# Optimization experiments

Measured on AMD Instinct MI355X. Metric: run time of the kernel, lower is better.

## Reference

```python
import jax, jax.numpy as jnp
import numpy as np

INPUT_DIM = 256
NODE_DIM = 6
OUTPUT_DIM = 256
N_NODES = 10000
N_EDGES = 320000


def setup_inputs() -> dict:
    key = jax.random.key(0)
    ks = jax.random.split(key, 6)
    x = jax.random.normal(ks[0], (N_NODES, NODE_DIM), dtype=jnp.float32)
    edge_index = jax.random.randint(ks[1], (2, N_EDGES), 0, N_NODES, dtype=jnp.int64 if jax.config.jax_enable_x64 else jnp.int32)
    edge_attr = jax.random.normal(ks[2], (N_EDGES, INPUT_DIM), dtype=jnp.float32)
    mask = jax.random.uniform(ks[3], (N_EDGES,), dtype=jnp.float32)
    in_feat = INPUT_DIM * 3 + NODE_DIM * 2  # 774
    limit = float(np.sqrt(6.0 / (in_feat + OUTPUT_DIM)))  # xavier_uniform
    W = jax.random.uniform(ks[4], (OUTPUT_DIM, in_feat), dtype=jnp.float32, minval=-limit, maxval=limit)
    b = jax.random.uniform(ks[5], (OUTPUT_DIM,), dtype=jnp.float32, minval=-1.0 / np.sqrt(in_feat), maxval=1.0 / np.sqrt(in_feat))
    return {"x": x, "num_nodes": N_NODES, "edge_index": edge_index, "edge_attr": edge_attr, "mask": mask, "W": W, "b": b}


def reference(x, num_nodes, edge_index, edge_attr, mask, W, b):
    row = edge_index[0]
    col = edge_index[1]
    # masked mean-ish aggregation of edge features into destination nodes
    num = jax.ops.segment_sum(edge_attr * mask[:, None], col, num_segments=num_nodes)  # [N, input_dim]
    den = jax.ops.segment_sum(mask[:, None], col, num_segments=num_nodes)             # [N, 1]
    node_rep = num / (den + 1.0)
    node_rep = jnp.concatenate([node_rep, x], axis=1)  # [N, input_dim + node_dim]
    edge_rep = jnp.concatenate([node_rep[row], node_rep[col], edge_attr], axis=-1)  # [E, 3*input_dim + 2*node_dim]
    edge_rep = edge_rep @ W.T + b  # [E, output_dim]
    return (node_rep, edge_rep)
```

## Files before the change

kernel.cpp:

```cpp
#include <hip/hip_runtime.h>
#include <hip/hip_bf16.h>
#include <stdint.h>

typedef __attribute__((ext_vector_type(4))) float f32x4;
typedef __attribute__((ext_vector_type(8))) short bf16x8;

#define NDIM 6
#define IN_DIM 256
#define OUT_DIM 256
#define KW 780
#define NR 262
#define NRP 320
#define SCAN_T 1024

__device__ __forceinline__ short f2bf(float f) {
  return __builtin_bit_cast(short, __float2bfloat16(f));
}

__device__ __forceinline__ void gload_lds16(void* lds, const void* g) {
  __builtin_amdgcn_global_load_lds(
      (const __attribute__((address_space(1))) unsigned int*)g,
      (__attribute__((address_space(3))) unsigned int*)lds, 16, 0, 0);
}

__global__ void hist_kernel(const int* __restrict__ ei, int* __restrict__ counts, int E) {
  int e = blockIdx.x * 256 + threadIdx.x;
  if (e < E) atomicAdd(&counts[ei[(long)E + e]], 1);
}

__global__ __launch_bounds__(SCAN_T) void scan_kernel(const int* __restrict__ counts,
                                                      int* __restrict__ offsets, int N) {
  __shared__ int part[SCAN_T];
  int t = threadIdx.x;
  int chunk = (N + SCAN_T - 1) / SCAN_T;
  int begin = t * chunk;
  int s = 0;
  for (int i = 0; i < chunk; ++i) {
    int idx = begin + i;
    if (idx < N) s += counts[idx];
  }
  part[t] = s;
  __syncthreads();
  for (int d = 1; d < SCAN_T; d <<= 1) {
    int v = (t >= d) ? part[t - d] : 0;
    __syncthreads();
    part[t] += v;
    __syncthreads();
  }
  int run = (t == 0) ? 0 : part[t - 1];
  for (int i = 0; i < chunk; ++i) {
    int idx = begin + i;
    if (idx < N) { offsets[idx] = run; run += counts[idx]; }
  }
}

__global__ void scatter_kernel(const int* __restrict__ ei, const int* __restrict__ offsets,
                               int* __restrict__ cursor, int* __restrict__ csr, int E) {
  int e = blockIdx.x * 256 + threadIdx.x;
  if (e >= E) return;
  int col = ei[(long)E + e];
  int pos = atomicAdd(&cursor[col], 1);
  csr[offsets[col] + pos] = e;
}

__global__ __launch_bounds__(256) void reduce_kernel(
    const int* __restrict__ csr, const int* __restrict__ offsets,
    const int* __restrict__ counts, const float* __restrict__ ea,
    const float* __restrict__ mask, const float* __restrict__ x,
    float* __restrict__ outN, short* __restrict__ nrepb, int N) {
  int n = blockIdx.x * 4 + (threadIdx.x >> 6);
  if (n >= N) return;
  int lane = threadIdx.x & 63;
  int s = offsets[n], cnt = counts[n];
  f32x4 sum = (f32x4)0.0f;
  float den = 0.0f;
#pragma unroll 4
  for (int i = 0; i < cnt; ++i) {
    int e = csr[s + i];
    float m = mask[e];
    den += m;
    f32x4 v = ((const f32x4*)ea)[(long)e * 64 + lane];
    sum.x += v.x * m; sum.y += v.y * m; sum.z += v.z * m; sum.w += v.w * m;
  }
  float inv = 1.0f / (den + 1.0f);
  sum.x *= inv; sum.y *= inv; sum.z *= inv; sum.w *= inv;
  float* po = outN + (long)n * NR + lane * 4;
  po[0] = sum.x; po[1] = sum.y; po[2] = sum.z; po[3] = sum.w;
  short4 pb;
  pb.x = f2bf(sum.x); pb.y = f2bf(sum.y); pb.z = f2bf(sum.z); pb.w = f2bf(sum.w);
  *(short4*)(nrepb + (long)n * NRP + lane * 4) = pb;
  if (lane < NDIM) {
    float xv = x[(long)n * NDIM + lane];
    outN[(long)n * NR + IN_DIM + lane] = xv;
    nrepb[(long)n * NRP + IN_DIM + lane] = f2bf(xv);
  } else if (lane < 8) {
    nrepb[(long)n * NRP + IN_DIM + lane] = 0;
  }
}

__global__ void wprep_kernel(const float* __restrict__ W, short* __restrict__ Weat,
                             short* __restrict__ Wrt, short* __restrict__ Wct) {
  int idx = blockIdx.x * 256 + threadIdx.x;
  if (idx < OUT_DIM * 256) {
    int n = idx >> 8, k = idx & 255;
    Weat[idx] = f2bf(W[(long)n * KW + 2 * NR + k]);
    return;
  }
  idx -= OUT_DIM * 256;
  if (idx < OUT_DIM * NRP) {
    int n = idx / NRP, k = idx % NRP;
    Wrt[idx] = f2bf(k < NR ? W[(long)n * KW + k] : 0.0f);
    return;
  }
  idx -= OUT_DIM * NRP;
  if (idx < OUT_DIM * NRP) {
    int n = idx / NRP, k = idx % NRP;
    Wct[idx] = f2bf(k < NR ? W[(long)n * KW + NR + k] : 0.0f);
  }
}

__global__ __launch_bounds__(256, 2) void pgemm_kernel(
    const short* __restrict__ nrepb, const short* __restrict__ Wrt,
    const short* __restrict__ Wct, const float* __restrict__ bias,
    float* __restrict__ Pr, float* __restrict__ Pc, int N) {
  __shared__ short As[5][64 * 64];
  const int tid = threadIdx.x;
  const int wave = tid >> 6, lane = tid & 63;
  const int m0 = blockIdx.x * 64;
  const int table = blockIdx.y;
  const short* Wt = table ? Wct : Wrt;
  float* P = table ? Pc : Pr;
  const int nbase = wave * 64;

  float bvals[4];
#pragma unroll
  for (int nf = 0; nf < 4; ++nf)
    bvals[nf] = table ? 0.0f : bias[nbase + 16 * nf + (lane & 15)];

  f32x4 acc[4][4];
#pragma unroll
  for (int mf = 0; mf < 4; ++mf)
#pragma unroll
    for (int nf = 0; nf < 4; ++nf) acc[mf][nf] = (f32x4)0.0f;

  bf16x8 bv[2][8];
  auto loadB = [&](int t, int tb) {
#pragma unroll
    for (int s2 = 0; s2 < 2; ++s2)
#pragma unroll
      for (int nf = 0; nf < 4; ++nf)
        bv[tb][s2 * 4 + nf] = *(const bf16x8*)&Wt[
            (long)(nbase + nf * 16 + (lane & 15)) * NRP + t * 64 + s2 * 32 + (lane >> 4) * 8];
  };

  const int scp = lane & 7;
#pragma unroll
  for (int t = 0; t < 5; ++t)
#pragma unroll
    for (int i = 0; i < 2; ++i) {
      int row = 16 * wave + 8 * i + (lane >> 3);
      int c = scp ^ (row & 7);
      long m = m0 + row; if (m >= N) m = N - 1;
      gload_lds16(&As[t][(16 * wave + 8 * i) * 64], nrepb + m * NRP + t * 64 + 8 * c);
    }
  loadB(0, 0);
  asm volatile("s_waitcnt vmcnt(8)" ::: "memory");
  __builtin_amdgcn_s_barrier();
  __builtin_amdgcn_sched_barrier(0);

#pragma unroll
  for (int t = 0; t < 5; ++t) {
    if (t < 4) loadB(t + 1, (t + 1) & 1);
    if (t < 4) asm volatile("s_waitcnt vmcnt(8)" ::: "memory");
    else       asm volatile("s_waitcnt vmcnt(0)" ::: "memory");
#pragma unroll
    for (int s2 = 0; s2 < 2; ++s2) {
      bf16x8 a[4];
      int cl = s2 * 4 + (lane >> 4);
#pragma unroll
      for (int mf = 0; mf < 4; ++mf) {
        int m = 16 * mf + (lane & 15);
        a[mf] = *(const bf16x8*)&As[t][m * 64 + ((cl ^ (m & 7)) * 8)];
      }
#pragma unroll
      for (int mf = 0; mf < 4; ++mf)
#pragma unroll
        for (int nf = 0; nf < 4; ++nf)
          acc[mf][nf] = __builtin_amdgcn_mfma_f32_16x16x32_bf16(
              a[mf], bv[t & 1][s2 * 4 + nf], acc[mf][nf], 0, 0, 0);
    }
  }

#pragma unroll
  for (int mf = 0; mf < 4; ++mf)
#pragma unroll
    for (int nf = 0; nf < 4; ++nf)
#pragma unroll
      for (int q = 0; q < 4; ++q) {
        long m = m0 + 16 * mf + (lane >> 4) * 4 + q;
        if (m < N)
          P[m * OUT_DIM + nbase + 16 * nf + (lane & 15)] = acc[mf][nf][q] + bvals[nf];
      }
}

__global__ __launch_bounds__(256, 2) void egemm_kernel(
    const int* __restrict__ ei, const float* __restrict__ ea,
    const short* __restrict__ Weat, const float* __restrict__ Pr,
    const float* __restrict__ Pc, float* __restrict__ outE, int E) {
  __shared__ short As[4][64 * 64];
  const int tid = threadIdx.x;
  const int wave = tid >> 6, lane = tid & 63;
  const long e0 = (long)blockIdx.x * 64;
  const int nbase = wave * 64;

  f32x4 acc[4][4];
#pragma unroll
  for (int mf = 0; mf < 4; ++mf)
#pragma unroll
    for (int nf = 0; nf < 4; ++nf) acc[mf][nf] = (f32x4)0.0f;

  bf16x8 bv[2][8];
  auto loadB = [&](int t, int tb) {
#pragma unroll
    for (int s2 = 0; s2 < 2; ++s2)
#pragma unroll
      for (int nf = 0; nf < 4; ++nf)
        bv[tb][s2 * 4 + nf] = *(const bf16x8*)&Weat[
            (nbase + nf * 16 + (lane & 15)) * 256 + t * 64 + s2 * 32 + (lane >> 4) * 8];
  };

  f32x4 eh[8][2];
#pragma unroll
  for (int j = 0; j < 8; ++j) {
    int c8 = tid + j * 256;
    int row = c8 >> 5, cp8 = c8 & 31;
    long e = e0 + row; if (e >= E) e = E - 1;
    const f32x4* s = (const f32x4*)(ea + (e * IN_DIM + cp8 * 8));
    eh[j][0] = s[0];
    eh[j][1] = s[1];
  }
  loadB(0, 0);
  __builtin_amdgcn_sched_barrier(0);
#pragma unroll
  for (int j = 0; j < 8; ++j) {
    int c8 = tid + j * 256;
    int row = c8 >> 5, cp8 = c8 & 31;
    int t = cp8 >> 3, cp = cp8 & 7;
    f32x4 v0 = eh[j][0], v1 = eh[j][1];
    bf16x8 p;
    p[0] = f2bf(v0.x); p[1] = f2bf(v0.y); p[2] = f2bf(v0.z); p[3] = f2bf(v0.w);
    p[4] = f2bf(v1.x); p[5] = f2bf(v1.y); p[6] = f2bf(v1.z); p[7] = f2bf(v1.w);
    *(bf16x8*)&As[t][row * 64 + ((cp ^ (row & 7)) * 8)] = p;
  }
  asm volatile("s_waitcnt lgkmcnt(0)" ::: "memory");
  __builtin_amdgcn_s_barrier();
  __builtin_amdgcn_sched_barrier(0);

#pragma unroll
  for (int t = 0; t < 4; ++t) {
    if (t < 3) loadB(t + 1, (t + 1) & 1);
    if (t < 3) asm volatile("s_waitcnt vmcnt(8)" ::: "memory");
    else       asm volatile("s_waitcnt vmcnt(0)" ::: "memory");
#pragma unroll
    for (int s2 = 0; s2 < 2; ++s2) {
      bf16x8 a[4];
      int cl = s2 * 4 + (lane >> 4);
#pragma unroll
      for (int mf = 0; mf < 4; ++mf) {
        int m = 16 * mf + (lane & 15);
        a[mf] = *(const bf16x8*)&As[t][m * 64 + ((cl ^ (m & 7)) * 8)];
      }
#pragma unroll
      for (int mf = 0; mf < 4; ++mf)
#pragma unroll
        for (int nf = 0; nf < 4; ++nf)
          acc[mf][nf] = __builtin_amdgcn_mfma_f32_16x16x32_bf16(
              a[mf], bv[t & 1][s2 * 4 + nf], acc[mf][nf], 0, 0, 0);
    }
  }

#pragma unroll
  for (int mf = 0; mf < 4; ++mf) {
#pragma unroll
    for (int q = 0; q < 4; ++q) {
      long e = e0 + 16 * mf + (lane >> 4) * 4 + q;
      bool ok = e < E;
      long ec = ok ? e : (E - 1);
      int re = ei[ec], ce = ei[(long)E + ec];
      const float* pr = Pr + (long)re * OUT_DIM;
      const float* pc = Pc + (long)ce * OUT_DIM;
      if (ok) {
#pragma unroll
        for (int nf = 0; nf < 4; ++nf) {
          int n = nbase + 16 * nf + (lane & 15);
          outE[e * OUT_DIM + n] = acc[mf][nf][q] + pr[n] + pc[n];
        }
      }
    }
  }
}

extern "C" void kernel_launch(void* const* d_in, const int* in_sizes, int n_in,
                              void* d_out, int out_size, void* d_ws, size_t ws_size,
                              hipStream_t stream) {
  const float* x    = (const float*)d_in[0];
  const int*   ei   = (const int*)d_in[2];
  const float* ea   = (const float*)d_in[3];
  const float* mask = (const float*)d_in[4];
  const float* W    = (const float*)d_in[5];
  const float* b    = (const float*)d_in[6];
  const int E = in_sizes[4];
  const int N = in_sizes[0] / NDIM;

  char* p = (char*)d_ws;
  int* counts  = (int*)p; p += (long)N * 4;
  int* cursor  = (int*)p; p += (long)N * 4;
  int* offsets = (int*)p; p += (long)(N + 1) * 4;
  int* csr     = (int*)p; p += (long)E * 4;
  p = (char*)(((uintptr_t)p + 15) & ~(uintptr_t)15);
  short* nrepb = (short*)p; p += (long)N * NRP * 2;
  short* Weat  = (short*)p; p += (long)OUT_DIM * 256 * 2;
  short* Wrt   = (short*)p; p += (long)OUT_DIM * NRP * 2;
  short* Wct   = (short*)p; p += (long)OUT_DIM * NRP * 2;
  float* Pr    = (float*)p; p += (long)N * OUT_DIM * 4;
  float* Pc    = (float*)p;

  float* outN = (float*)d_out;
  float* outE = outN + (long)N * NR;

  hipMemsetAsync(counts, 0, (size_t)2 * N * 4, stream);

  hist_kernel<<<(E + 255) / 256, 256, 0, stream>>>(ei, counts, E);
  scan_kernel<<<1, SCAN_T, 0, stream>>>(counts, offsets, N);
  scatter_kernel<<<(E + 255) / 256, 256, 0, stream>>>(ei, offsets, cursor, csr, E);
  reduce_kernel<<<(N + 3) / 4, 256, 0, stream>>>(csr, offsets, counts, ea, mask, x,
                                                 outN, nrepb, N);
  int wtot = OUT_DIM * 256 + 2 * OUT_DIM * NRP;
  wprep_kernel<<<(wtot + 255) / 256, 256, 0, stream>>>(W, Weat, Wrt, Wct);
  dim3 pg((N + 63) / 64, 2);
  pgemm_kernel<<<pg, 256, 0, stream>>>(nrepb, Wrt, Wct, b, Pr, Pc, N);
  egemm_kernel<<<(E + 63) / 64, 256, 0, stream>>>(ei, ea, Weat, Pr, Pc, outE, E);
}
```

Baseline: 392.0 us.

## Store node projection tables in bf16 and batch CSR index loads in reduce

The per-node projection tables Pr and Pc are now written and read as bf16 instead of fp32. This halves the bytes of the random row gathers in the edge GEMM epilogue and the writes in the node GEMM. The reduce kernel now loads 64 edge indices and masks at once, one per lane, and broadcasts them with readlane, prefetching the next chunk. This shortens the dependent index-then-mask-then-data chain per edge. Bf16 storage adds rounding error to the summed output, which sits on top of the bf16 GEMM operands already in use.

```diff
diff --git a/kernel.cpp b/kernel.cpp
--- a/kernel.cpp
+++ b/kernel.cpp
@@ -15,6 +15,10 @@
 
 __device__ __forceinline__ short f2bf(float f) {
   return __builtin_bit_cast(short, __float2bfloat16(f));
+}
+__device__ __forceinline__ float bf2f(short h) {
+  unsigned int u = ((unsigned int)(unsigned short)h) << 16;
+  return __builtin_bit_cast(float, u);
 }
 
 __device__ __forceinline__ void gload_lds16(void* lds, const void* g) {
@@ -74,14 +78,29 @@
   int s = offsets[n], cnt = counts[n];
   f32x4 sum = (f32x4)0.0f;
   float den = 0.0f;
-#pragma unroll 4
-  for (int i = 0; i < cnt; ++i) {
-    int e = csr[s + i];
-    float m = mask[e];
-    den += m;
-    f32x4 v = ((const f32x4*)ea)[(long)e * 64 + lane];
-    sum.x += v.x * m; sum.y += v.y * m; sum.z += v.z * m; sum.w += v.w * m;
-  }
+
+  int ecur = 0; float mcur = 0.0f;
+  if (lane < cnt) { ecur = csr[s + lane]; mcur = mask[ecur]; }
+
+  for (int base = 0; base < cnt; base += 64) {
+    int enext = 0; float mnext = 0.0f;
+    if (base + 64 < cnt) {
+      int idx = base + 64 + lane;
+      if (idx < cnt) { enext = csr[s + idx]; mnext = mask[enext]; }
+    }
+    int mbits = __builtin_bit_cast(int, mcur);
+#pragma unroll
+    for (int i = 0; i < 64; ++i) {
+      if (base + i >= cnt) break;
+      int e = __builtin_amdgcn_readlane(ecur, i);
+      float m = __builtin_bit_cast(float, __builtin_amdgcn_readlane(mbits, i));
+      f32x4 v = ((const f32x4*)ea)[(long)e * 64 + lane];
+      sum.x += v.x * m; sum.y += v.y * m; sum.z += v.z * m; sum.w += v.w * m;
+      den += m;
+    }
+    ecur = enext; mcur = mnext;
+  }
+
   float inv = 1.0f / (den + 1.0f);
   sum.x *= inv; sum.y *= inv; sum.z *= inv; sum.w *= inv;
   float* po = outN + (long)n * NR + lane * 4;
@@ -122,14 +141,14 @@
 __global__ __launch_bounds__(256, 2) void pgemm_kernel(
     const short* __restrict__ nrepb, const short* __restrict__ Wrt,
     const short* __restrict__ Wct, const float* __restrict__ bias,
-    float* __restrict__ Pr, float* __restrict__ Pc, int N) {
+    short* __restrict__ Pr, short* __restrict__ Pc, int N) {
   __shared__ short As[5][64 * 64];
   const int tid = threadIdx.x;
   const int wave = tid >> 6, lane = tid & 63;
   const int m0 = blockIdx.x * 64;
   const int table = blockIdx.y;
   const short* Wt = table ? Wct : Wrt;
-  float* P = table ? Pc : Pr;
+  short* P = table ? Pc : Pr;
   const int nbase = wave * 64;
 
   float bvals[4];
@@ -199,14 +218,14 @@
       for (int q = 0; q < 4; ++q) {
         long m = m0 + 16 * mf + (lane >> 4) * 4 + q;
         if (m < N)
-          P[m * OUT_DIM + nbase + 16 * nf + (lane & 15)] = acc[mf][nf][q] + bvals[nf];
+          P[m * OUT_DIM + nbase + 16 * nf + (lane & 15)] = f2bf(acc[mf][nf][q] + bvals[nf]);
       }
 }
 
 __global__ __launch_bounds__(256, 2) void egemm_kernel(
     const int* __restrict__ ei, const float* __restrict__ ea,
-    const short* __restrict__ Weat, const float* __restrict__ Pr,
-    const float* __restrict__ Pc, float* __restrict__ outE, int E) {
+    const short* __restrict__ Weat, const short* __restrict__ Pr,
+    const short* __restrict__ Pc, float* __restrict__ outE, int E) {
   __shared__ short As[4][64 * 64];
   const int tid = threadIdx.x;
   const int wave = tid >> 6, lane = tid & 63;
@@ -287,13 +306,13 @@
       bool ok = e < E;
       long ec = ok ? e : (E - 1);
       int re = ei[ec], ce = ei[(long)E + ec];
-      const float* pr = Pr + (long)re * OUT_DIM;
-      const float* pc = Pc + (long)ce * OUT_DIM;
+      const short* pr = Pr + (long)re * OUT_DIM;
+      const short* pc = Pc + (long)ce * OUT_DIM;
       if (ok) {
 #pragma unroll
         for (int nf = 0; nf < 4; ++nf) {
           int n = nbase + 16 * nf + (lane & 15);
-          outE[e * OUT_DIM + n] = acc[mf][nf][q] + pr[n] + pc[n];
+          outE[e * OUT_DIM + n] = acc[mf][nf][q] + bf2f(pr[n]) + bf2f(pc[n]);
         }
       }
     }
@@ -322,8 +341,8 @@
   short* Weat  = (short*)p; p += (long)OUT_DIM * 256 * 2;
   short* Wrt   = (short*)p; p += (long)OUT_DIM * NRP * 2;
   short* Wct   = (short*)p; p += (long)OUT_DIM * NRP * 2;
-  float* Pr    = (float*)p; p += (long)N * OUT_DIM * 4;
-  float* Pc    = (float*)p;
+  short* Pr    = (short*)p; p += (long)N * OUT_DIM * 2;
+  short* Pc    = (short*)p;
 
   float* outN = (float*)d_out;
   float* outE = outN + (long)N * NR;
```

Result: faster. 383.9 us (median of 2 runs) (-2.1%).
